# Performance work log

Hardware: AMD Instinct MI355X
Metric: run time of the kernel (lower is better)

## Reference

```python
import jax, jax.numpy as jnp
import numpy as np

B, T, C, H = 4, 2048, 1024, 16
HD = C // H


def setup_inputs() -> dict:
    key = jax.random.key(0)
    ks = jax.random.split(key, 9)
    s = 1.0 / np.sqrt(C)
    return {
        "x": jax.random.normal(ks[0], (B, T, C), dtype=jnp.float32),
        "Wk": jax.random.uniform(ks[1], (C, C), jnp.float32, -s, s),
        "bk": jax.random.uniform(ks[2], (C,), jnp.float32, -s, s),
        "Wq": jax.random.uniform(ks[3], (C, C), jnp.float32, -s, s),
        "bq": jax.random.uniform(ks[4], (C,), jnp.float32, -s, s),
        "Wv": jax.random.uniform(ks[5], (C, C), jnp.float32, -s, s),
        "bv": jax.random.uniform(ks[6], (C,), jnp.float32, -s, s),
        "Wp": jax.random.uniform(ks[7], (C, C), jnp.float32, -s, s),
        "bp": jax.random.uniform(ks[8], (C,), jnp.float32, -s, s),
        "padding_mask": jnp.ones((B, T), dtype=jnp.int32),
    }


def reference(x, Wk, bk, Wq, bq, Wv, bv, Wp, bp, padding_mask):
    # torch nn.Linear: y = x @ W.T + b  (W is [out, in])
    def split_heads(t):  # [B,T,C] -> [B,H,T,HD]
        return t.reshape(B, T, H, HD).transpose(0, 2, 1, 3)

    k = split_heads(x @ Wk.T + bk)
    q = split_heads(x @ Wq.T + bq)
    v = split_heads(x @ Wv.T + bv)

    scale = 1.0 / jnp.sqrt(jnp.float32(HD))
    att = jnp.einsum("bhqd,bhkd->bhqk", q, k) * scale  # [B,H,T,T]

    causal = jnp.tril(jnp.ones((T, T), dtype=bool))  # [T,T]
    pad = (padding_mask != 0)[:, None, None, :]       # [B,1,1,T]
    mask = causal[None, None, :, :] & pad
    att = jnp.where(mask, att, -jnp.inf)
    att = jax.nn.softmax(att, axis=-1)

    y = jnp.einsum("bhqk,bhkd->bhqd", att, v)  # [B,H,T,HD]
    y = y.transpose(0, 2, 1, 3).reshape(B, T, C)
    return y @ Wp.T + bp
```

## Files before the change

kernel.cpp:

```cpp
#include <hip/hip_runtime.h>
#include <hip/hip_bf16.h>
#include <math.h>
#include <stdint.h>

#define BB 4
#define TT 2048
#define CC 1024
#define HH 16
#define HD 64
#define MM (BB*TT)
#define NQT 8
#define SCQ 0.180336878f

using f32x4  = __attribute__((ext_vector_type(4))) float;
using f32x16 = __attribute__((ext_vector_type(16))) float;
using i32x4  = __attribute__((ext_vector_type(4))) int;
using bf16x4 = __attribute__((ext_vector_type(4))) __bf16;
using bf16x8 = __attribute__((ext_vector_type(8))) __bf16;

__device__ __forceinline__ float fast_exp2(float x) {
  return __builtin_amdgcn_exp2f(x);
}

__device__ __forceinline__ int cvt_pk_bf16(float lo, float hi_) {
  int r;
  asm("v_cvt_pk_bf16_f32 %0, %1, %2" : "=v"(r) : "v"(lo), "v"(hi_));
  return r;
}

__device__ __forceinline__ void gload_lds16(const void* g, void* l) {
  __builtin_amdgcn_global_load_lds(
      (__attribute__((address_space(1))) void*)(void*)(g),
      (__attribute__((address_space(3))) void*)(l), 16, 0, 0);
}

__global__ __launch_bounds__(256)
void cvt_f32_bf16(const float* __restrict__ s, __bf16* __restrict__ d, int n4) {
  int i = blockIdx.x * 256 + threadIdx.x;
  if (i >= n4) return;
  float4 v = ((const float4*)s)[i];
  bf16x4 o;
  o[0] = (__bf16)v.x; o[1] = (__bf16)v.y; o[2] = (__bf16)v.z; o[3] = (__bf16)v.w;
  *(bf16x4*)(d + (size_t)i * 4) = o;
}

__global__ __launch_bounds__(256)
void cvt_w4(const float* __restrict__ Wq, const float* __restrict__ Wk,
            const float* __restrict__ Wv, const float* __restrict__ Wp,
            __bf16* __restrict__ wqkv, __bf16* __restrict__ wpb) {
  int which = blockIdx.y;
  const float* s = which == 0 ? Wq : which == 1 ? Wk : which == 2 ? Wv : Wp;
  __bf16* d = which == 3 ? wpb : wqkv + (size_t)which * CC * CC;
  float sc = which == 0 ? SCQ : 1.f;
  int i = blockIdx.x * 256 + threadIdx.x;
  float4 v = ((const float4*)s)[i];
  bf16x4 o;
  o[0] = (__bf16)(v.x * sc); o[1] = (__bf16)(v.y * sc);
  o[2] = (__bf16)(v.z * sc); o[3] = (__bf16)(v.w * sc);
  *(bf16x4*)(d + (size_t)i * 4) = o;
}

#define WAITV6 asm volatile("s_waitcnt vmcnt(6)" ::: "memory")
#define WAITV0 asm volatile("s_waitcnt vmcnt(0)" ::: "memory")
#define WAITL0 asm volatile("s_waitcnt lgkmcnt(0)" ::: "memory")
#define BARR   __builtin_amdgcn_s_barrier()
#define SB0    __builtin_amdgcn_sched_barrier(0)
#define PRIO1  __builtin_amdgcn_s_setprio(1)
#define PRIO0  __builtin_amdgcn_s_setprio(0)

#define LDA_SET(buf, mq)                                                      \
  {                                                                           \
    const char* base_ = (const char*)&LA[buf][mq][0] + (wm * 64 + lq) * 128;  \
    _Pragma("unroll")                                                         \
    for (int m4 = 0; m4 < 4; ++m4)                                            \
      _Pragma("unroll")                                                       \
      for (int kk = 0; kk < 2; ++kk)                                          \
        a[m4 * 2 + kk] =                                                      \
            *(const bf16x8*)(base_ + m4 * 2048 + ((kk * 64 + g * 16) ^ swz)); \
  }

#define LDB_SET(buf, nq)                                                      \
  {                                                                           \
    const char* base_ = (const char*)&LB[buf][nq][0] + (wn * 32 + lq) * 128;  \
    _Pragma("unroll")                                                         \
    for (int n2 = 0; n2 < 2; ++n2)                                            \
      _Pragma("unroll")                                                       \
      for (int kk = 0; kk < 2; ++kk)                                          \
        b[nq][n2 * 2 + kk] =                                                  \
            *(const bf16x8*)(base_ + n2 * 2048 + ((kk * 64 + g * 16) ^ swz)); \
  }

#define STAGE_A(nbuf, h, tt)                                                  \
  {                                                                           \
    const char* s_ = Ag + ((size_t)((h)*128 + srow)) * 2048 + (tt)*128 + scol1; \
    gload_lds16(s_, (char*)&LA[nbuf][h][0] + so16);                           \
    gload_lds16(s_ + (size_t)64 * 2048, (char*)&LA[nbuf][h][0] + so16 + 8192);\
  }

#define STAGE_B(nbuf, h, tt)                                                  \
  {                                                                           \
    const char* s_ = Bg + ((size_t)((h)*128 + srow)) * 2048 + (tt)*128 + scol1; \
    gload_lds16(s_, (char*)&LB[nbuf][h][0] + so16);                           \
    gload_lds16(s_ + (size_t)64 * 2048, (char*)&LB[nbuf][h][0] + so16 + 8192);\
  }

#define MFMA_PH(mq, nq)                                                       \
  _Pragma("unroll")                                                           \
  for (int m4 = 0; m4 < 4; ++m4)                                              \
    _Pragma("unroll")                                                         \
    for (int n2 = 0; n2 < 2; ++n2)                                            \
      _Pragma("unroll")                                                       \
      for (int kk = 0; kk < 2; ++kk)                                          \
        acc[mq][m4][nq][n2] = __builtin_amdgcn_mfma_f32_16x16x32_bf16(        \
            a[m4 * 2 + kk], b[nq][n2 * 2 + kk], acc[mq][m4][nq][n2], 0, 0, 0);

__global__ __launch_bounds__(512, 2)
void gemm_qkv(const __bf16* __restrict__ A, const __bf16* __restrict__ Bm,
              const float* __restrict__ b0, const float* __restrict__ b1,
              const float* __restrict__ b2, __bf16* __restrict__ out,
              __bf16* __restrict__ vt) {
  __shared__ __bf16 LA[2][2][128 * 64];
  __shared__ __bf16 LB[2][2][128 * 64];
  const int tid = threadIdx.x, wid = tid >> 6, lane = tid & 63;
  const int g = lane >> 4, lq = lane & 15;
  const int wm = wid >> 2, wn = wid & 3;
  const int bm = blockIdx.x / 12, bn = blockIdx.x % 12;
  const int brow = bm << 8, bcol = bn << 8;
  const int swz = (lq & 7) << 4;

  const int srow = tid >> 3, so16 = tid * 16;
  const int scol1 = ((tid & 7) << 4) ^ ((srow & 7) << 4);
  const char* Ag = (const char*)A + (size_t)brow * 2048;
  const char* Bg = (const char*)Bm + (size_t)bcol * 2048;

  f32x4 acc[2][4][2][2] = {};
  bf16x8 a[8], b[2][4];

  STAGE_A(0, 0, 0); STAGE_B(0, 0, 0); STAGE_B(0, 1, 0); STAGE_A(0, 1, 0);
  STAGE_A(1, 0, 1); STAGE_B(1, 0, 1); STAGE_B(1, 1, 1);
  WAITV6; BARR;

#pragma unroll 1
  for (int t = 0; t < 8; ++t) {
    const bool s2 = (t < 7);
    const int k1 = 2 * t + 1, k2 = 2 * t + 2, k3 = 2 * t + 3;
    LDA_SET(0, 0); LDB_SET(0, 0);
    STAGE_A(1, 1, k1);
    BARR; WAITL0; SB0;
    PRIO1; MFMA_PH(0, 0); PRIO0; BARR;
    LDB_SET(0, 1);
    if (s2) STAGE_A(0, 0, k2);
    BARR; WAITL0; SB0;
    PRIO1; MFMA_PH(0, 1); PRIO0; BARR;
    LDA_SET(0, 1);
    if (s2) STAGE_B(0, 0, k2);
    BARR; WAITL0; SB0;
    PRIO1; MFMA_PH(1, 1); PRIO0; BARR;
    if (s2) { STAGE_B(0, 1, k2); WAITV6; } else { WAITV0; }
    BARR; SB0;
    PRIO1; MFMA_PH(1, 0); PRIO0; BARR;
    LDA_SET(1, 0); LDB_SET(1, 0);
    if (s2) STAGE_A(0, 1, k2);
    BARR; WAITL0; SB0;
    PRIO1; MFMA_PH(0, 0); PRIO0; BARR;
    LDB_SET(1, 1);
    if (s2) STAGE_A(1, 0, k3);
    BARR; WAITL0; SB0;
    PRIO1; MFMA_PH(0, 1); PRIO0; BARR;
    LDA_SET(1, 1);
    if (s2) STAGE_B(1, 0, k3);
    BARR; WAITL0; SB0;
    PRIO1; MFMA_PH(1, 1); PRIO0; BARR;
    if (s2) { STAGE_B(1, 1, k3); WAITV6; }
    BARR; SB0;
    PRIO1; MFMA_PH(1, 0); PRIO0; BARR;
  }

  const int proj = bn >> 2;
  if (proj < 2) {
    const float* bias = proj == 0 ? b0 : b1;
    const float bsc = proj == 0 ? SCQ : 1.f;
#pragma unroll
    for (int mq = 0; mq < 2; ++mq)
#pragma unroll
      for (int nq = 0; nq < 2; ++nq)
#pragma unroll
        for (int n2 = 0; n2 < 2; ++n2) {
          int col = bcol + nq * 128 + wn * 32 + n2 * 16 + lq;
          int cw = col & (CC - 1);
          float bb = bias[cw] * bsc;
          int h_ = cw >> 6, d_ = cw & (HD - 1);
#pragma unroll
          for (int m4 = 0; m4 < 4; ++m4) {
            int row0 = brow + mq * 128 + wm * 64 + m4 * 16 + g * 4;
#pragma unroll
            for (int i = 0; i < 4; ++i) {
              int row = row0 + i;
              int b_ = row >> 11, t_ = row & (TT - 1);
              out[((size_t)proj << 23) +
                  ((((size_t)b_ * HH + h_) * TT + t_) << 6) + d_] =
                  (__bf16)(acc[mq][m4][nq][n2][i] + bb);
            }
          }
        }
  } else {
    __bf16* lt = (__bf16*)&LA[0][0][0];
    const int cv0 = (bn & 3) << 8;
    const int b_ = brow >> 11, t0 = brow & (TT - 1);
    const int hbase = (bn & 3) << 2;
    const int rd_d = tid >> 3, rd_tb = (tid & 7) << 5;
#pragma unroll
    for (int cc = 0; cc < 4; ++cc) {
      if ((wn >> 1) == (cc & 1)) {
#pragma unroll
        for (int n2 = 0; n2 < 2; ++n2) {
          int c = ((wn & 1) << 5) + (n2 << 4) + lq;
          float bb = b2[cv0 + (cc << 6) + c];
#pragma unroll
          for (int mq = 0; mq < 2; ++mq)
#pragma unroll
            for (int m4 = 0; m4 < 4; ++m4) {
              int r = (mq << 7) + (wm << 6) + (m4 << 4) + (g << 2);
              bf16x4 pk;
#pragma unroll
              for (int i = 0; i < 4; ++i)
                pk[i] = (__bf16)(acc[mq][m4][cc >> 1][n2][i] + bb);
              *(bf16x4*)(lt + c * 264 + r) = pk;
            }
        }
      }
      __syncthreads();
      __bf16* dst = vt + (((size_t)((b_ * HH + hbase + cc) * HD + rd_d)) << 11)
                       + t0 + rd_tb;
      const __bf16* srcl = lt + rd_d * 264 + rd_tb;
#pragma unroll
      for (int j = 0; j < 4; ++j)
        *(bf16x8*)(dst + j * 8) = *(const bf16x8*)(srcl + j * 8);
      __syncthreads();
    }
  }
}

__global__ __launch_bounds__(256, 2)
void gemm_proj(const __bf16* __restrict__ A, const __bf16* __restrict__ Bm,
               const float* __restrict__ bias, float* __restrict__ out,
               int M, int N, int K) {
  __shared__ __bf16 As[128 * 32];
  __shared__ __bf16 Bs[128 * 32];
  const int tid = threadIdx.x;
  const int wid = tid >> 6, lane = tid & 63;
  const int g = lane >> 4, lq = lane & 15;
  const int nbn = N >> 7;
  const int brow = (blockIdx.x / nbn) << 7;
  const int bcol = (blockIdx.x % nbn) << 7;
  const int wr = (wid >> 1) << 6, wc = (wid & 1) << 6;

  f32x4 acc[4][4] = {};

  const int o0 = wid * 2048 + lane * 16;
  for (int kt = 0; kt < K; kt += 32) {
    __syncthreads();
#pragma unroll
    for (int j = 0; j < 2; ++j) {
      int o = o0 + j * 1024;
      int row = o >> 6, colb = o & 63;
      gload_lds16((const char*)A + ((size_t)(brow + row) * K + kt) * 2 + colb,
                  (char*)As + o);
      gload_lds16((const char*)Bm + ((size_t)(bcol + row) * K + kt) * 2 + colb,
                  (char*)Bs + o);
    }
    __syncthreads();
    bf16x8 av[4], bv[4];
#pragma unroll
    for (int m = 0; m < 4; ++m)
      av[m] = *(const bf16x8*)(As + (wr + m * 16 + lq) * 32 + g * 8);
#pragma unroll
    for (int n = 0; n < 4; ++n)
      bv[n] = *(const bf16x8*)(Bs + (wc + n * 16 + lq) * 32 + g * 8);
#pragma unroll
    for (int m = 0; m < 4; ++m)
#pragma unroll
      for (int n = 0; n < 4; ++n)
        acc[m][n] = __builtin_amdgcn_mfma_f32_16x16x32_bf16(av[m], bv[n], acc[m][n], 0, 0, 0);
  }

#pragma unroll
  for (int m = 0; m < 4; ++m) {
#pragma unroll
    for (int n = 0; n < 4; ++n) {
      int col = bcol + wc + n * 16 + lq;
      float bb = bias[col];
      int row0 = brow + wr + m * 16 + g * 4;
#pragma unroll
      for (int i = 0; i < 4; ++i)
        out[(size_t)(row0 + i) * N + col] = acc[m][n][i] + bb;
    }
  }
}

__global__ __launch_bounds__(512, 4)
void attn_fwd(const __bf16* __restrict__ Q, const __bf16* __restrict__ K,
              const __bf16* __restrict__ Vt, const int* __restrict__ pm,
              __bf16* __restrict__ Y) {
  __shared__ __bf16 Ks[2][64 * 64];
  __shared__ __bf16 Vs[2][64 * 64];
  const int tid = threadIdx.x, wid = tid >> 6, lane = tid & 63;
  const int l31 = lane & 31, hi = lane >> 5;
  const int bx = blockIdx.x;
  const int bh = bx & 63, jj = bx >> 6;
  const int r2 = ((jj & 1) << 1) | ((jj >> 1) & 1);
  const int qi = (jj & 4) ? r2 : 7 - r2;
  const int b_ = bh >> 4, h_ = bh & 15;
  const __bf16* Qb = Q + (size_t)bh * TT * HD;
  const __bf16* Kb = K + (size_t)bh * TT * HD;
  const __bf16* Vb = Vt + (size_t)bh * HD * TT;
  const int* pmb = pm + b_ * TT;

  const int so = tid * 16;
  const int srow = so >> 7, scol = (so & 127) ^ ((srow & 7) << 4);

  const int q0 = qi << 8;
  const int qw = q0 + wid * 32;
  const int ntiles = 4 * qi + 4;
  const int sw0 = (l31 & 7) << 4;

  bf16x8 qf[4];
#pragma unroll
  for (int s = 0; s < 4; ++s)
    qf[s] = *(const bf16x8*)(Qb + (size_t)(qw + l31) * HD + s * 16 + hi * 8);

  f32x16 o0 = {}, o1 = {};
  float lsum = 0.f;
  float m = -INFINITY;

  gload_lds16((const char*)Kb + (size_t)srow * 128 + scol, (char*)&Ks[0][0] + so);
  gload_lds16((const char*)Vb + (size_t)srow * (TT * 2) + scol, (char*)&Vs[0][0] + so);
  __syncthreads();

  int cur = 0;
#pragma unroll 1
  for (int t = 0; t < ntiles; ++t) {
    const int kv0 = t << 6;
    const int pmv = pmb[kv0 + lane];
    if (t + 1 < ntiles) {
      const size_t nkv0 = (size_t)(kv0 + 64);
      gload_lds16((const char*)Kb + (nkv0 + srow) * 128 + scol,
                  (char*)&Ks[cur ^ 1][0] + so);
      gload_lds16((const char*)Vb + (size_t)srow * (TT * 2) + nkv0 * 2 + scol,
                  (char*)&Vs[cur ^ 1][0] + so);
    }

    if (kv0 <= qw + 31) {
      unsigned long long bits = __ballot(pmv != 0);

      const char* KsC = (const char*)&Ks[cur][0];
      f32x16 sA = {}, sB = {};
      __builtin_amdgcn_s_setprio(1);
#pragma unroll
      for (int s = 0; s < 4; ++s) {
        const int co = 32 * s + 16 * hi;
        bf16x8 k0 = *(const bf16x8*)(KsC + l31 * 128 + (co ^ sw0));
        bf16x8 k1 = *(const bf16x8*)(KsC + (32 + l31) * 128 + (co ^ sw0));
        sA = __builtin_amdgcn_mfma_f32_32x32x16_bf16(k0, qf[s], sA, 0, 0, 0);
        sB = __builtin_amdgcn_mfma_f32_32x32x16_bf16(k1, qf[s], sB, 0, 0, 0);
      }
      __builtin_amdgcn_s_setprio(0);

      const bool diag = (kv0 + 63 > qw);
      const bool nopad = (bits == ~0ull);
      if (__builtin_expect(!nopad, 0)) {
#pragma unroll
        for (int r = 0; r < 16; ++r) {
          const int c = (r & 3) + 8 * (r >> 2);
          if (!((bits >> (c + 4 * hi)) & 1ull)) sA[r] = -INFINITY;
          if (!((bits >> (32 + c + 4 * hi)) & 1ull)) sB[r] = -INFINITY;
        }
      }
      if (diag) {
        const int thr = qw + l31 - kv0 - 4 * hi;
#pragma unroll
        for (int r = 0; r < 16; ++r) {
          const int c = (r & 3) + 8 * (r >> 2);
          sA[r] = (c <= thr) ? sA[r] : -INFINITY;
          sB[r] = (32 + c <= thr) ? sB[r] : -INFINITY;
        }
      }

      float mx[8];
#pragma unroll
      for (int r = 0; r < 8; ++r)
        mx[r] = fmaxf(fmaxf(sA[r], sA[r + 8]), fmaxf(sB[r], sB[r + 8]));
#pragma unroll
      for (int r = 0; r < 4; ++r) mx[r] = fmaxf(mx[r], mx[r + 4]);
      float pmax = fmaxf(fmaxf(mx[0], mx[1]), fmaxf(mx[2], mx[3]));

      const bool ok = (pmax <= m + 8.f);
      if (!__all(ok)) {
        float nm = fmaxf(pmax, __shfl_xor(pmax, 32));
        float mn = fmaxf(m, nm);
        float c = fast_exp2(m - mn);
        m = mn;
        lsum *= c;
#pragma unroll
        for (int r = 0; r < 16; ++r) {
          float cr = __shfl(c, (r & 3) + 8 * (r >> 2) + 4 * hi);
          o0[r] *= cr;
          o1[r] *= cr;
        }
      }

#pragma unroll
      for (int r = 0; r < 16; ++r) sA[r] = fast_exp2(sA[r] - m);
#pragma unroll
      for (int r = 0; r < 16; ++r) sB[r] = fast_exp2(sB[r] - m);
      {
        float sm[8];
#pragma unroll
        for (int r = 0; r < 8; ++r)
          sm[r] = (sA[r] + sA[r + 8]) + (sB[r] + sB[r + 8]);
#pragma unroll
        for (int r = 0; r < 4; ++r) sm[r] += sm[r + 4];
        lsum += (sm[0] + sm[1]) + (sm[2] + sm[3]);
      }

      const char* VsC = (const char*)&Vs[cur][0];
      __builtin_amdgcn_s_setprio(1);
#pragma unroll
      for (int s = 0; s < 4; ++s) {
        const f32x16& P = (s < 2) ? sA : sB;
        const int ub = 2 * (s & 1);
        int A0 = cvt_pk_bf16(P[4 * ub + 0], P[4 * ub + 1]);
        int A1 = cvt_pk_bf16(P[4 * ub + 2], P[4 * ub + 3]);
        int B0 = cvt_pk_bf16(P[4 * ub + 4], P[4 * ub + 5]);
        int B1 = cvt_pk_bf16(P[4 * ub + 6], P[4 * ub + 7]);
        int s0 = hi ? A0 : B0, s1 = hi ? A1 : B1;
        int e0 = __shfl_xor(s0, 32), e1 = __shfl_xor(s1, 32);
        i32x4 wv;
        wv[0] = hi ? e0 : A0;
        wv[1] = hi ? e1 : A1;
        wv[2] = hi ? B0 : e0;
        wv[3] = hi ? B1 : e1;
        bf16x8 pa = __builtin_bit_cast(bf16x8, wv);
        const int co = 32 * s + 16 * hi;
        bf16x8 v0 = *(const bf16x8*)(VsC + l31 * 128 + (co ^ sw0));
        bf16x8 v1 = *(const bf16x8*)(VsC + (32 + l31) * 128 + (co ^ sw0));
        o0 = __builtin_amdgcn_mfma_f32_32x32x16_bf16(pa, v0, o0, 0, 0, 0);
        o1 = __builtin_amdgcn_mfma_f32_32x32x16_bf16(pa, v1, o1, 0, 0, 0);
      }
      __builtin_amdgcn_s_setprio(0);
    }

    __syncthreads();
    cur ^= 1;
  }

  float linv = 1.f / (lsum + __shfl_xor(lsum, 32));
#pragma unroll
  for (int r = 0; r < 16; ++r) {
    const int crow = (r & 3) + 8 * (r >> 2) + 4 * hi;
    float ir = __shfl(linv, crow);
    const int qrow = qw + crow;
    __bf16* yp = Y + ((size_t)(b_ * TT + qrow)) * CC + h_ * HD + l31;
    yp[0]  = (__bf16)(o0[r] * ir);
    yp[32] = (__bf16)(o1[r] * ir);
  }
}

extern "C" void kernel_launch(void* const* d_in, const int* in_sizes, int n_in,
                              void* d_out, int out_size, void* d_ws, size_t ws_size,
                              hipStream_t stream) {
  (void)in_sizes; (void)n_in; (void)out_size; (void)ws_size;
  const float* x  = (const float*)d_in[0];
  const float* Wk = (const float*)d_in[1];
  const float* bk = (const float*)d_in[2];
  const float* Wq = (const float*)d_in[3];
  const float* bq = (const float*)d_in[4];
  const float* Wv = (const float*)d_in[5];
  const float* bv = (const float*)d_in[6];
  const float* Wp = (const float*)d_in[7];
  const float* bp = (const float*)d_in[8];
  const int* pmask = (const int*)d_in[9];

  char* ws = (char*)d_ws;
  const size_t MB = 1024 * 1024;
  __bf16* xb   = (__bf16*)(ws);
  __bf16* wqkv = (__bf16*)(ws + 16 * MB);
  __bf16* wpb  = (__bf16*)(ws + 22 * MB);
  __bf16* qb   = (__bf16*)(ws + 24 * MB);
  __bf16* kb   = qb + ((size_t)1 << 23);
  __bf16* vtb  = (__bf16*)(ws + 56 * MB);
  __bf16* yb   = xb;

  int n4 = (MM * CC) / 4;
  cvt_f32_bf16<<<(n4 + 255) / 256, 256, 0, stream>>>(x, xb, n4);
  cvt_w4<<<dim3((CC * CC / 4) / 256, 4), 256, 0, stream>>>(
      Wq, Wk, Wv, Wp, wqkv, wpb);

  gemm_qkv<<<(MM / 256) * (3 * CC / 256), 512, 0, stream>>>(
      xb, wqkv, bq, bk, bv, qb, vtb);

  attn_fwd<<<NQT * BB * HH, 512, 0, stream>>>(qb, kb, vtb, pmask, yb);

  gemm_proj<<<(MM / 128) * (CC / 128), 256, 0, stream>>>(
      yb, wpb, bp, (float*)d_out, MM, CC, CC);
}
```

Measured before the change: 182.5 us.

## Split attention KV tile into 32-key halves and skip fully masked half

Processes each 64-key tile as two 32-key halves, each doing its own QK MFMA, masking, online-softmax update and PV MFMA. The upper half is skipped when it lies entirely above the causal diagonal, which removes wasted work on diagonal tiles, and the live score registers drop from two 16-wide accumulators to one. The cost is more serialization: the max/rescale check and its shuffles now run twice per tile, and a sched_barrier limits how the compiler can interleave the two halves.

```diff
diff --git a/kernel.cpp b/kernel.cpp
--- a/kernel.cpp
+++ b/kernel.cpp
@@ -351,103 +351,94 @@
     }
 
     if (kv0 <= qw + 31) {
-      unsigned long long bits = __ballot(pmv != 0);
-
-      const char* KsC = (const char*)&Ks[cur][0];
-      f32x16 sA = {}, sB = {};
-      __builtin_amdgcn_s_setprio(1);
-#pragma unroll
-      for (int s = 0; s < 4; ++s) {
-        const int co = 32 * s + 16 * hi;
-        bf16x8 k0 = *(const bf16x8*)(KsC + l31 * 128 + (co ^ sw0));
-        bf16x8 k1 = *(const bf16x8*)(KsC + (32 + l31) * 128 + (co ^ sw0));
-        sA = __builtin_amdgcn_mfma_f32_32x32x16_bf16(k0, qf[s], sA, 0, 0, 0);
-        sB = __builtin_amdgcn_mfma_f32_32x32x16_bf16(k1, qf[s], sB, 0, 0, 0);
-      }
-      __builtin_amdgcn_s_setprio(0);
-
-      const bool diag = (kv0 + 63 > qw);
-      const bool nopad = (bits == ~0ull);
-      if (__builtin_expect(!nopad, 0)) {
-#pragma unroll
-        for (int r = 0; r < 16; ++r) {
-          const int c = (r & 3) + 8 * (r >> 2);
-          if (!((bits >> (c + 4 * hi)) & 1ull)) sA[r] = -INFINITY;
-          if (!((bits >> (32 + c + 4 * hi)) & 1ull)) sB[r] = -INFINITY;
+      const unsigned long long bits = __ballot(pmv != 0);
+      const char* VsC = (const char*)&Vs[cur][0];
+
+#pragma unroll
+      for (int h = 0; h < 2; ++h) {
+        const int kvh = kv0 + 32 * h;
+        if (kvh <= qw + 31) {
+          const char* KsC = (const char*)&Ks[cur][0] + (32 * h + l31) * 128;
+          f32x16 S = {};
+          __builtin_amdgcn_s_setprio(1);
+#pragma unroll
+          for (int s = 0; s < 4; ++s) {
+            bf16x8 kf = *(const bf16x8*)(KsC + ((32 * s + 16 * hi) ^ sw0));
+            S = __builtin_amdgcn_mfma_f32_32x32x16_bf16(kf, qf[s], S, 0, 0, 0);
+          }
+          __builtin_amdgcn_s_setprio(0);
+
+          if (__builtin_expect(bits != ~0ull, 0)) {
+#pragma unroll
+            for (int r = 0; r < 16; ++r) {
+              const int c = (r & 3) + 8 * (r >> 2);
+              if (!((bits >> (32 * h + c + 4 * hi)) & 1ull)) S[r] = -INFINITY;
+            }
+          }
+          if (kvh + 31 > qw) {
+            const int thr = qw + l31 - kvh - 4 * hi;
+#pragma unroll
+            for (int r = 0; r < 16; ++r) {
+              const int c = (r & 3) + 8 * (r >> 2);
+              S[r] = (c <= thr) ? S[r] : -INFINITY;
+            }
+          }
+
+          float t0 = fmaxf(fmaxf(S[0], S[1]), fmaxf(S[2], S[3]));
+          float t1 = fmaxf(fmaxf(S[4], S[5]), fmaxf(S[6], S[7]));
+          float t2 = fmaxf(fmaxf(S[8], S[9]), fmaxf(S[10], S[11]));
+          float t3 = fmaxf(fmaxf(S[12], S[13]), fmaxf(S[14], S[15]));
+          float pmax = fmaxf(fmaxf(t0, t1), fmaxf(t2, t3));
+          if (!__all(pmax <= m + 8.f)) {
+            float nm = fmaxf(pmax, __shfl_xor(pmax, 32));
+            float mn = fmaxf(m, nm);
+            float c = fast_exp2(m - mn);
+            m = mn;
+            lsum *= c;
+#pragma unroll
+            for (int r = 0; r < 16; ++r) {
+              float cr = __shfl(c, (r & 3) + 8 * (r >> 2) + 4 * hi);
+              o0[r] *= cr;
+              o1[r] *= cr;
+            }
+          }
+
+#pragma unroll
+          for (int r = 0; r < 16; ++r) S[r] = fast_exp2(S[r] - m);
+          {
+            float u0 = (S[0] + S[1]) + (S[2] + S[3]);
+            float u1 = (S[4] + S[5]) + (S[6] + S[7]);
+            float u2 = (S[8] + S[9]) + (S[10] + S[11]);
+            float u3 = (S[12] + S[13]) + (S[14] + S[15]);
+            lsum += (u0 + u1) + (u2 + u3);
+          }
+
+          __builtin_amdgcn_s_setprio(1);
+#pragma unroll
+          for (int s = 0; s < 2; ++s) {
+            const int ub = 2 * s;
+            int A0 = cvt_pk_bf16(S[4 * ub + 0], S[4 * ub + 1]);
+            int A1 = cvt_pk_bf16(S[4 * ub + 2], S[4 * ub + 3]);
+            int B0 = cvt_pk_bf16(S[4 * ub + 4], S[4 * ub + 5]);
+            int B1 = cvt_pk_bf16(S[4 * ub + 6], S[4 * ub + 7]);
+            int s0 = hi ? A0 : B0, s1 = hi ? A1 : B1;
+            int e0 = __shfl_xor(s0, 32), e1 = __shfl_xor(s1, 32);
+            i32x4 wv;
+            wv[0] = hi ? e0 : A0;
+            wv[1] = hi ? e1 : A1;
+            wv[2] = hi ? B0 : e0;
+            wv[3] = hi ? B1 : e1;
+            bf16x8 pa = __builtin_bit_cast(bf16x8, wv);
+            const int co = 64 * h + 32 * s + 16 * hi;
+            bf16x8 v0 = *(const bf16x8*)(VsC + l31 * 128 + (co ^ sw0));
+            bf16x8 v1 = *(const bf16x8*)(VsC + (32 + l31) * 128 + (co ^ sw0));
+            o0 = __builtin_amdgcn_mfma_f32_32x32x16_bf16(pa, v0, o0, 0, 0, 0);
+            o1 = __builtin_amdgcn_mfma_f32_32x32x16_bf16(pa, v1, o1, 0, 0, 0);
+          }
+          __builtin_amdgcn_s_setprio(0);
+          __builtin_amdgcn_sched_barrier(0);
         }
       }
-      if (diag) {
-        const int thr = qw + l31 - kv0 - 4 * hi;
-#pragma unroll
-        for (int r = 0; r < 16; ++r) {
-          const int c = (r & 3) + 8 * (r >> 2);
-          sA[r] = (c <= thr) ? sA[r] : -INFINITY;
-          sB[r] = (32 + c <= thr) ? sB[r] : -INFINITY;
-        }
-      }
-
-      float mx[8];
-#pragma unroll
-      for (int r = 0; r < 8; ++r)
-        mx[r] = fmaxf(fmaxf(sA[r], sA[r + 8]), fmaxf(sB[r], sB[r + 8]));
-#pragma unroll
-      for (int r = 0; r < 4; ++r) mx[r] = fmaxf(mx[r], mx[r + 4]);
-      float pmax = fmaxf(fmaxf(mx[0], mx[1]), fmaxf(mx[2], mx[3]));
-
-      const bool ok = (pmax <= m + 8.f);
-      if (!__all(ok)) {
-        float nm = fmaxf(pmax, __shfl_xor(pmax, 32));
-        float mn = fmaxf(m, nm);
-        float c = fast_exp2(m - mn);
-        m = mn;
-        lsum *= c;
-#pragma unroll
-        for (int r = 0; r < 16; ++r) {
-          float cr = __shfl(c, (r & 3) + 8 * (r >> 2) + 4 * hi);
-          o0[r] *= cr;
-          o1[r] *= cr;
-        }
-      }
-
-#pragma unroll
-      for (int r = 0; r < 16; ++r) sA[r] = fast_exp2(sA[r] - m);
-#pragma unroll
-      for (int r = 0; r < 16; ++r) sB[r] = fast_exp2(sB[r] - m);
-      {
-        float sm[8];
-#pragma unroll
-        for (int r = 0; r < 8; ++r)
-          sm[r] = (sA[r] + sA[r + 8]) + (sB[r] + sB[r + 8]);
-#pragma unroll
-        for (int r = 0; r < 4; ++r) sm[r] += sm[r + 4];
-        lsum += (sm[0] + sm[1]) + (sm[2] + sm[3]);
-      }
-
-      const char* VsC = (const char*)&Vs[cur][0];
-      __builtin_amdgcn_s_setprio(1);
-#pragma unroll
-      for (int s = 0; s < 4; ++s) {
-        const f32x16& P = (s < 2) ? sA : sB;
-        const int ub = 2 * (s & 1);
-        int A0 = cvt_pk_bf16(P[4 * ub + 0], P[4 * ub + 1]);
-        int A1 = cvt_pk_bf16(P[4 * ub + 2], P[4 * ub + 3]);
-        int B0 = cvt_pk_bf16(P[4 * ub + 4], P[4 * ub + 5]);
-        int B1 = cvt_pk_bf16(P[4 * ub + 6], P[4 * ub + 7]);
-        int s0 = hi ? A0 : B0, s1 = hi ? A1 : B1;
-        int e0 = __shfl_xor(s0, 32), e1 = __shfl_xor(s1, 32);
-        i32x4 wv;
-        wv[0] = hi ? e0 : A0;
-        wv[1] = hi ? e1 : A1;
-        wv[2] = hi ? B0 : e0;
-        wv[3] = hi ? B1 : e1;
-        bf16x8 pa = __builtin_bit_cast(bf16x8, wv);
-        const int co = 32 * s + 16 * hi;
-        bf16x8 v0 = *(const bf16x8*)(VsC + l31 * 128 + (co ^ sw0));
-        bf16x8 v1 = *(const bf16x8*)(VsC + (32 + l31) * 128 + (co ^ sw0));
-        o0 = __builtin_amdgcn_mfma_f32_32x32x16_bf16(pa, v0, o0, 0, 0, 0);
-        o1 = __builtin_amdgcn_mfma_f32_32x32x16_bf16(pa, v1, o1, 0, 0, 0);
-      }
-      __builtin_amdgcn_s_setprio(0);
     }
 
     __syncthreads();
```

New measurement: 180.7 us. No clear change (-1.0%).
